# Performance work log

Hardware: AMD Instinct MI355X
Metric: run time of the kernel (lower is better)

The kernel has to match this reference:

```python
import jax, jax.numpy as jnp
import numpy as np

B, S, D = 1, 2048, 128   # batch, seq_len, num_hidden (== head dim)
H, KVH = 32, 8           # num_heads, num_kv_heads
REP = H // KVH           # num_rep = 4
D_K = 128                # softmax scale denominator sqrt(d_k)
ROPE_THETA = 10000.0


def _rope(x):
    # x: (B, h, S, D). Standard rotate-half RoPE over last dim, positions on axis -2.
    inv_freq = 1.0 / (ROPE_THETA ** (jnp.arange(0, D, 2, dtype=jnp.float32) / D))  # (D/2,)
    ang = jnp.arange(S, dtype=jnp.float32)[:, None] * inv_freq                      # (S, D/2)
    cos = jnp.concatenate([jnp.cos(ang), jnp.cos(ang)], axis=-1)                    # (S, D)
    sin = jnp.concatenate([jnp.sin(ang), jnp.sin(ang)], axis=-1)
    x1, x2 = jnp.split(x, 2, axis=-1)
    rot = jnp.concatenate([-x2, x1], axis=-1)
    return x * cos + rot * sin


def setup_inputs() -> dict:
    key = jax.random.key(0)
    ks = jax.random.split(key, 11)
    w = 0.02
    return {
        "query":  jax.random.normal(ks[0], (B, S, D), jnp.float32),
        "keys":   jax.random.normal(ks[1], (B, S, D), jnp.float32),
        "values": jax.random.normal(ks[2], (B, S, D), jnp.float32),
        "Wq": jax.random.normal(ks[3], (D, H * D), jnp.float32) * w,
        "bq": jnp.zeros((H * D,), jnp.float32),
        "Wk": jax.random.normal(ks[4], (D, KVH * D), jnp.float32) * w,
        "bk": jnp.zeros((KVH * D,), jnp.float32),
        "Wv": jax.random.normal(ks[5], (D, KVH * D), jnp.float32) * w,
        "bv": jnp.zeros((KVH * D,), jnp.float32),
        "Wo": jax.random.normal(ks[6], (H * D, D), jnp.float32) * w,
        "bo": jnp.zeros((D,), jnp.float32),
    }


def reference(query, keys, values, Wq, bq, Wk, bk, Wv, bv, Wo, bo):
    # Projections; faithful to torch .view(): plain reshape (B,S,h*D)->(B,h,S,D), no transpose.
    q = (query @ Wq + bq).reshape(B, H, S, D)
    k = (keys @ Wk + bk).reshape(B, KVH, S, D)
    v = (values @ Wv + bv).reshape(B, KVH, S, D)
    k = _rope(k)
    v = _rope(v)  # module applies RoPE to values too
    # torch repeat tiles kv heads: q head i <-> kv head (i % KVH).
    qg = q.reshape(B, REP, KVH, S, D)
    scores = jnp.einsum('brgsd,bgtd->brgst', qg, k) / jnp.sqrt(jnp.float32(D_K))
    attn = jax.nn.softmax(scores, axis=-1)  # mask=False path, no causal mask
    out = jnp.einsum('brgst,bgtd->brgsd', attn, v).reshape(B, H, S, D)
    out = out.transpose(0, 2, 1, 3).reshape(B, S, H * D)
    return out @ Wo + bo
```

## Files before the change

### kernel.cpp

```cpp
#include <hip/hip_runtime.h>
#include <math.h>


#define SCALE_L2E 0.12751878222550723f
#define L2_10K_64 0.20762050593045952f

typedef short bf16x8 __attribute__((ext_vector_type(8)));
typedef float f32x4 __attribute__((ext_vector_type(4)));
typedef float f32x16 __attribute__((ext_vector_type(16)));

__device__ __forceinline__ unsigned short f2b(float f) {
  union { float f; unsigned u; } x; x.f = f;
  return (unsigned short)((x.u + 0x7FFFu + ((x.u >> 16) & 1u)) >> 16);
}
__device__ __forceinline__ float b2f(unsigned short b) {
  union { unsigned u; float f; } x; x.u = ((unsigned)b) << 16;
  return x.f;
}
__device__ __forceinline__ void lds_dma16(void* lds, const void* g) {
  __builtin_amdgcn_global_load_lds(
      (const __attribute__((address_space(1))) unsigned int*)g,
      (__attribute__((address_space(3))) unsigned int*)lds, 16, 0, 0);
}
__device__ __forceinline__ unsigned cvtpk(float lo, float hi) {
  unsigned r;
  asm("v_cvt_pk_bf16_f32 %0, %1, %2" : "=v"(r) : "v"(lo), "v"(hi));
  return r;
}
#define PLSWAP(a, b) asm("v_permlane32_swap_b32 %0, %1" : "+v"(a), "+v"(b))

__device__ __forceinline__ void redist(unsigned pw[8], bf16x8* f0, bf16x8* f1) {
  PLSWAP(pw[0], pw[2]); PLSWAP(pw[1], pw[3]);
  PLSWAP(pw[4], pw[6]); PLSWAP(pw[5], pw[7]);
  union { unsigned u[4]; bf16x8 v; } a, b;
  a.u[0] = pw[0]; a.u[1] = pw[1]; a.u[2] = pw[2]; a.u[3] = pw[3];
  b.u[0] = pw[4]; b.u[1] = pw[5]; b.u[2] = pw[6]; b.u[3] = pw[7];
  *f0 = a.v; *f1 = b.v;
}

__global__ __launch_bounds__(256) void prep_weights(
    const float* __restrict__ Wk, const float* __restrict__ Wv,
    const float* __restrict__ Wo, const float* __restrict__ Wq,
    unsigned short* __restrict__ Wkt, unsigned short* __restrict__ Wvt,
    unsigned short* __restrict__ Wot, unsigned short* __restrict__ Wq2) {
  __shared__ unsigned short T[64][66];
  int b = blockIdx.x, tid = threadIdx.x;
  const float* W;
  unsigned short* D;
  int K, N, tk, tn;
  if (b < 32) {
    W = Wk; D = Wkt; K = 128; N = 1024; int ti = b;       tk = ti & 1;  tn = ti >> 1;
  } else if (b < 64) {
    W = Wv; D = Wvt; K = 128; N = 1024; int ti = b - 32;  tk = ti & 1;  tn = ti >> 1;
  } else if (b < 192) {
    W = Wo; D = Wot; K = 4096; N = 128; int ti = b - 64;  tk = ti >> 1; tn = ti & 1;
  } else {
    int i0 = ((b - 192) * 256 + tid) * 16;
#pragma unroll
    for (int j = 0; j < 16; ++j) Wq2[i0 + j] = f2b(Wq[i0 + j]);
    return;
  }
  int k0 = tk * 64, n0 = tn * 64;
  int c = tid & 63, q = tid >> 6;
#pragma unroll
  for (int i = 0; i < 16; ++i) {
    int r = i * 4 + q;
    T[r][c] = f2b(W[(size_t)(k0 + r) * N + n0 + c]);
  }
  __syncthreads();
#pragma unroll
  for (int i = 0; i < 16; ++i) {
    int r = i * 4 + q;
    D[(size_t)(n0 + r) * K + k0 + c] = T[c][r];
  }
}

__global__ __launch_bounds__(256) void proj_kv(
    const float* __restrict__ keys, const float* __restrict__ values,
    const unsigned short* __restrict__ Wkt, const unsigned short* __restrict__ Wvt,
    const float* __restrict__ bk, const float* __restrict__ bv,
    unsigned short* __restrict__ kp, unsigned short* __restrict__ vt) {
  int bx = blockIdx.x, m0 = blockIdx.y * 64;
  int tid = threadIdx.x;
  int w = tid >> 6, l = tid & 63;
  int l16 = l & 15, g4 = l >> 4;
  int arow = m0 + w * 16 + l16;
  const f32x4 fz = {0.f, 0.f, 0.f, 0.f};
  int vmode = bx >> 3;
  int n0 = (bx & 7) * 128, tb = bx & 7;
  const float* X = vmode ? values : keys;
  const unsigned short* Wt = vmode ? Wvt : Wkt;
  const float* bias = vmode ? bv : bk;
  f32x4 acc[8];
#pragma unroll
  for (int nb = 0; nb < 8; ++nb) acc[nb] = fz;
#pragma unroll
  for (int kc = 0; kc < 4; ++kc) {
    int kbase = kc * 32 + g4 * 8;
    const float* xp = X + (size_t)arow * 128 + kbase;
    bf16x8 a;
#pragma unroll
    for (int j = 0; j < 8; ++j) a[j] = (short)f2b(xp[j]);
#pragma unroll
    for (int nb = 0; nb < 8; ++nb) {
      bf16x8 b = *(const bf16x8*)(Wt + (size_t)(n0 + nb * 16 + l16) * 128 + kbase);
      acc[nb] = __builtin_amdgcn_mfma_f32_16x16x32_bf16(a, b, acc[nb], 0, 0, 0);
    }
  }
#pragma unroll
  for (int nb = 0; nb < 4; ++nb) {
    int d2 = nb * 16 + l16;
    float invf = exp2f(-(float)d2 * L2_10K_64);
    float blo = bias[n0 + d2], bhi = bias[n0 + d2 + 64];
#pragma unroll
    for (int r = 0; r < 4; ++r) {
      int mi = m0 + w * 16 + g4 * 4 + r;
      int t = (mi & 255) * 8 + tb;
      float ang = (float)t * invf;
      float sf, cf;
      __sincosf(ang, &sf, &cf);
      float x1 = acc[nb][r] + blo;
      float x2 = acc[nb + 4][r] + bhi;
      unsigned short lo = f2b(x1 * cf - x2 * sf);
      unsigned short hi = f2b(x2 * cf + x1 * sf);
      int g = mi >> 8;
      if (vmode) {
        vt[(size_t)g * 262144 + (size_t)d2 * 2048 + t] = lo;
        vt[(size_t)g * 262144 + (size_t)(d2 + 64) * 2048 + t] = hi;
      } else {
        kp[(size_t)g * 262144 + (size_t)t * 128 + d2] = lo;
        kp[(size_t)g * 262144 + (size_t)t * 128 + d2 + 64] = hi;
      }
    }
  }
}

__global__ void ws_marker(float* __restrict__ out) {
  out[blockIdx.x * 256 + threadIdx.x] = 12345.0f;
}

__global__ void reduce_out(const float* __restrict__ part, const float* __restrict__ bo,
                           float* __restrict__ out) {
  int idx = blockIdx.x * 256 + threadIdx.x;
  float s = bo[idx & 127];
#pragma unroll
  for (int g = 0; g < 8; ++g) s += part[(size_t)g * 262144 + idx];
  out[idx] = s;
}

__global__ __launch_bounds__(256, 2) void attn_kernel(
    const float* __restrict__ X, const unsigned short* __restrict__ Wqb,
    const float* __restrict__ bq,
    const unsigned short* __restrict__ kp, const unsigned short* __restrict__ vt,
    const unsigned short* __restrict__ Wot, float* __restrict__ part) {
  __shared__ __align__(16) char smem[65536];
  int bid = blockIdx.x;
  int g = bid & 7;
  int qi0 = (bid >> 3) * 32;
  int q5 = qi0 >> 5;
  int tid = threadIdx.x;
  int w = tid >> 6, l = tid & 63;
  int l31 = l & 31, hi = l >> 5;
  int hw = g + 8 * w;

  const f32x16 fz16 = {0.f};

  {
    unsigned short* Uni = (unsigned short*)smem;
    int col0 = tid * 16;
#pragma unroll
    for (int jp = 0; jp < 2; ++jp) {
      float acc[2][16];
#pragma unroll
      for (int j = 0; j < 2; ++j)
#pragma unroll
        for (int cc = 0; cc < 16; ++cc) acc[j][cc] = bq[col0 + cc];
      const float* xr0 = X + (size_t)((g + 8 * (jp * 2)) * 64 + q5) * 128;
      const float* xr1 = X + (size_t)((g + 8 * (jp * 2 + 1)) * 64 + q5) * 128;
      for (int k = 0; k < 128; ++k) {
        float x0 = xr0[k], x1 = xr1[k];
        bf16x8 w0 = *(const bf16x8*)(Wqb + (size_t)k * 4096 + col0);
        bf16x8 w1 = *(const bf16x8*)(Wqb + (size_t)k * 4096 + col0 + 8);
#pragma unroll
        for (int e = 0; e < 8; ++e) {
          float f0 = b2f((unsigned short)w0[e]), f1 = b2f((unsigned short)w1[e]);
          acc[0][e] += x0 * f0; acc[0][8 + e] += x0 * f1;
          acc[1][e] += x1 * f0; acc[1][8 + e] += x1 * f1;
        }
      }
#pragma unroll
      for (int j = 0; j < 2; ++j)
#pragma unroll
        for (int cc = 0; cc < 16; ++cc)
          Uni[(jp * 2 + j) * 4096 + col0 + cc] = f2b(acc[j][cc]);
    }
  }
  __syncthreads();
  bf16x8 qfrag[8];
  {
    unsigned short* Uni = (unsigned short*)smem;
#pragma unroll
    for (int kc = 0; kc < 8; ++kc)
      qfrag[kc] = *(const bf16x8*)&Uni[w * 4096 + l31 * 128 + kc * 16 + hi * 8];
  }
  __syncthreads();

  const char* kg = (const char*)(kp + (size_t)g * 262144);
  const char* vg = (const char*)(vt + (size_t)g * 262144);

#define STAGE_K(tn, kb)                                                         \
  {                                                                             \
    _Pragma("unroll") for (int i = 0; i < 4; ++i) {                             \
      int off = w * 4096 + i * 1024 + l * 16;                                   \
      int row = off >> 8, ch = (off >> 4) & 15;                                 \
      int rch = ch ^ (row & 15);                                                \
      lds_dma16(smem + (kb) * 16384 + w * 4096 + i * 1024,                      \
                kg + (size_t)(tn) * 16384 + (size_t)row * 256 + rch * 16);      \
    }                                                                           \
  }
#define STAGE_V(tn, vb)                                                         \
  {                                                                             \
    _Pragma("unroll") for (int i = 0; i < 4; ++i) {                             \
      int off = w * 4096 + i * 1024 + l * 16;                                   \
      int row = off >> 7, ch = (off >> 4) & 7;                                  \
      int rch = ch ^ (row & 7);                                                 \
      lds_dma16(smem + 32768 + (vb) * 16384 + w * 4096 + i * 1024,              \
                vg + (size_t)row * 4096 + (size_t)(tn) * 128 + rch * 16);       \
    }                                                                           \
  }

  STAGE_K(0, 0);
  STAGE_V(0, 0);
  __syncthreads();

  f32x16 oacc[4];
#pragma unroll
  for (int db = 0; db < 4; ++db) oacc[db] = fz16;
  float lacc = 0.f;

  int c = 0;
  for (int t = 0; t < 32; ++t) {
    if (t < 31) { STAGE_K(t + 1, c ^ 1); STAGE_V(t + 1, c ^ 1); }

#pragma unroll
    for (int jb = 0; jb < 2; ++jb) {
      f32x16 sacc = fz16;
      __builtin_amdgcn_s_setprio(1);
#pragma unroll
      for (int kc = 0; kc < 8; ++kc) {
        int row = jb * 32 + l31;
        int rch = (kc * 2 + hi) ^ (row & 15);
        bf16x8 kfrag = *(const bf16x8*)(smem + c * 16384 + row * 256 + rch * 16);
        sacc = __builtin_amdgcn_mfma_f32_32x32x16_bf16(kfrag, qfrag[kc], sacc, 0, 0, 0);
      }
      __builtin_amdgcn_s_setprio(0);
      float p[16];
#pragma unroll
      for (int j = 0; j < 16; ++j) {
        p[j] = exp2f(sacc[j] * SCALE_L2E);
        lacc += p[j];
      }
      unsigned pw[8];
#pragma unroll
      for (int m = 0; m < 8; ++m) pw[m] = cvtpk(p[2 * m], p[2 * m + 1]);
      bf16x8 pf0, pf1;
      redist(pw, &pf0, &pf1);
      __builtin_amdgcn_s_setprio(1);
#pragma unroll
      for (int ks = 0; ks < 2; ++ks) {
        int ksg = jb * 2 + ks;
        bf16x8 pf = ks ? pf1 : pf0;
#pragma unroll
        for (int db = 0; db < 4; ++db) {
          int row = db * 32 + l31;
          int rch = (ksg * 2 + hi) ^ (row & 7);
          bf16x8 vfrag = *(const bf16x8*)(smem + 32768 + c * 16384 + row * 128 + rch * 16);
          oacc[db] = __builtin_amdgcn_mfma_f32_32x32x16_bf16(vfrag, pf, oacc[db], 0, 0, 0);
        }
      }
      __builtin_amdgcn_s_setprio(0);
    }
    __syncthreads();
    c ^= 1;
  }

  float ltot = lacc + __shfl_xor(lacc, 32, 64);
  float invl = 1.f / ltot;

  f32x16 acc2[4];
#pragma unroll
  for (int nb = 0; nb < 4; ++nb) acc2[nb] = fz16;
  bf16x8 ofrag[8];
#pragma unroll
  for (int db = 0; db < 4; ++db) {
    unsigned pw[8];
#pragma unroll
    for (int m = 0; m < 8; ++m)
      pw[m] = cvtpk(oacc[db][2 * m] * invl, oacc[db][2 * m + 1] * invl);
    redist(pw, &ofrag[db * 2], &ofrag[db * 2 + 1]);
  }
#pragma unroll
  for (int ks = 0; ks < 8; ++ks) {
#pragma unroll
    for (int nb = 0; nb < 4; ++nb) {
      bf16x8 wof = *(const bf16x8*)(Wot + (size_t)(nb * 32 + l31) * 4096 + hw * 128 + ks * 16 + hi * 8);
      acc2[nb] = __builtin_amdgcn_mfma_f32_32x32x16_bf16(wof, ofrag[ks], acc2[nb], 0, 0, 0);
    }
  }
  __syncthreads();
  float* Psum = (float*)(smem + w * 16384);
#pragma unroll
  for (int nb = 0; nb < 4; ++nb) {
#pragma unroll
    for (int j = 0; j < 16; ++j) {
      int no = nb * 32 + (j & 3) + 8 * (j >> 2) + 4 * hi;
      Psum[l31 * 128 + no] = acc2[nb][j];
    }
  }
  __syncthreads();
  {
    float* P0 = (float*)smem;
    float* dst = part + (size_t)g * 262144 + (size_t)qi0 * 128;
#pragma unroll
    for (int i = 0; i < 16; ++i) {
      int cidx = i * 256 + tid;
      dst[cidx] = P0[cidx] + P0[4096 + cidx] + P0[8192 + cidx] + P0[12288 + cidx];
    }
  }
#undef STAGE_K
#undef STAGE_V
}

extern "C" void kernel_launch(void* const* d_in, const int* in_sizes, int n_in,
                              void* d_out, int out_size, void* d_ws, size_t ws_size,
                              hipStream_t stream) {
  const float* query  = (const float*)d_in[0];
  const float* keys   = (const float*)d_in[1];
  const float* values = (const float*)d_in[2];
  const float* Wq = (const float*)d_in[3];
  const float* bq = (const float*)d_in[4];
  const float* Wk = (const float*)d_in[5];
  const float* bk = (const float*)d_in[6];
  const float* Wv = (const float*)d_in[7];
  const float* bv = (const float*)d_in[8];
  const float* Wo = (const float*)d_in[9];
  const float* bo = (const float*)d_in[10];
  float* out = (float*)d_out;
  char* ws = (char*)d_ws;
  const size_t MB = 1024 * 1024;
  const size_t NEED = 18 * MB + 512 * 1024;
  if (ws_size < NEED) {
    ws_marker<<<1024, 256, 0, stream>>>(out);
    return;
  }
  unsigned short* Wq2   = (unsigned short*)(ws);
  unsigned short* Wkt   = (unsigned short*)(ws + 1 * MB);
  unsigned short* Wvt   = (unsigned short*)(ws + 1 * MB + 256 * 1024);
  unsigned short* Wot   = (unsigned short*)(ws + 1 * MB + 512 * 1024);
  unsigned short* kproj = (unsigned short*)(ws + 2 * MB + 512 * 1024);
  unsigned short* vt    = (unsigned short*)(ws + 6 * MB + 512 * 1024);
  float* part           = (float*)(ws + 10 * MB + 512 * 1024);

  prep_weights<<<320, 256, 0, stream>>>(Wk, Wv, Wo, Wq, Wkt, Wvt, Wot, Wq2);
  proj_kv<<<dim3(16, 32), 256, 0, stream>>>(keys, values, Wkt, Wvt, bk, bv, kproj, vt);
  attn_kernel<<<512, 256, 0, stream>>>(query, Wq2, bq, kproj, vt, Wot, part);
  reduce_out<<<1024, 256, 0, stream>>>(part, bo, out);
}
```

Before: 171.5 us.

## Split attention KV loop across wave pairs and add separate MFMA Q projection

The attention kernel grows to 512 threads, and each pair of waves splits the two 32-key halves of every KV tile. Partial outputs and row sums from the two waves are merged through LDS before the output projection. K and V staging is divided between the two groups of waves. When the workspace is large enough, the Q projection moves from scalar FMA inside the attention kernel to a separate MFMA-based proj_q kernel that writes a bf16 Q buffer, at the cost of an extra launch and a 16MB intermediate.

```diff
diff --git a/kernel.cpp b/kernel.cpp
--- a/kernel.cpp
+++ b/kernel.cpp
@@ -42,7 +42,7 @@
     const float* __restrict__ Wk, const float* __restrict__ Wv,
     const float* __restrict__ Wo, const float* __restrict__ Wq,
     unsigned short* __restrict__ Wkt, unsigned short* __restrict__ Wvt,
-    unsigned short* __restrict__ Wot, unsigned short* __restrict__ Wq2) {
+    unsigned short* __restrict__ Wot, unsigned short* __restrict__ Wq2, int big) {
   __shared__ unsigned short T[64][66];
   int b = blockIdx.x, tid = threadIdx.x;
   const float* W;
@@ -55,10 +55,13 @@
   } else if (b < 192) {
     W = Wo; D = Wot; K = 4096; N = 128; int ti = b - 64;  tk = ti >> 1; tn = ti & 1;
   } else {
-    int i0 = ((b - 192) * 256 + tid) * 16;
-#pragma unroll
-    for (int j = 0; j < 16; ++j) Wq2[i0 + j] = f2b(Wq[i0 + j]);
-    return;
+    if (!big) {
+      int i0 = ((b - 192) * 256 + tid) * 16;
+#pragma unroll
+      for (int j = 0; j < 16; ++j) Wq2[i0 + j] = f2b(Wq[i0 + j]);
+      return;
+    }
+    W = Wq; D = Wq2; K = 128; N = 4096; int ti = b - 192; tk = ti & 1;  tn = ti >> 1;
   }
   int k0 = tk * 64, n0 = tn * 64;
   int c = tid & 63, q = tid >> 6;
@@ -135,6 +138,46 @@
   }
 }
 
+__global__ __launch_bounds__(256) void proj_q(const float* __restrict__ X,
+                                              const unsigned short* __restrict__ Wqt,
+                                              const float* __restrict__ bq,
+                                              unsigned short* __restrict__ qp) {
+  int n0 = blockIdx.x * 64, m0 = blockIdx.y * 64;
+  int tid = threadIdx.x;
+  int w = tid >> 6, l = tid & 63;
+  int l16 = l & 15, g4 = l >> 4;
+  int arow = m0 + w * 16 + l16;
+  const f32x4 fz = {0.f, 0.f, 0.f, 0.f};
+  f32x4 acc[4];
+#pragma unroll
+  for (int nb = 0; nb < 4; ++nb) acc[nb] = fz;
+#pragma unroll
+  for (int kc = 0; kc < 4; ++kc) {
+    int kbase = kc * 32 + g4 * 8;
+    const float* xp = X + (size_t)arow * 128 + kbase;
+    bf16x8 a;
+#pragma unroll
+    for (int j = 0; j < 8; ++j) a[j] = (short)f2b(xp[j]);
+#pragma unroll
+    for (int nb = 0; nb < 4; ++nb) {
+      bf16x8 b = *(const bf16x8*)(Wqt + (size_t)(n0 + nb * 16 + l16) * 128 + kbase);
+      acc[nb] = __builtin_amdgcn_mfma_f32_16x16x32_bf16(a, b, acc[nb], 0, 0, 0);
+    }
+  }
+#pragma unroll
+  for (int nb = 0; nb < 4; ++nb) {
+    int n = n0 + nb * 16 + l16;
+    float bvv = bq[n];
+#pragma unroll
+    for (int r = 0; r < 4; ++r) {
+      int mi = m0 + w * 16 + g4 * 4 + r;
+      int h = mi >> 6;
+      int s = ((mi & 63) << 5) | (n >> 7);
+      qp[((size_t)h * 2048 + s) * 128 + (n & 127)] = f2b(acc[nb][r] + bvv);
+    }
+  }
+}
+
 __global__ void ws_marker(float* __restrict__ out) {
   out[blockIdx.x * 256 + threadIdx.x] = 12345.0f;
 }
@@ -148,12 +191,13 @@
   out[idx] = s;
 }
 
-__global__ __launch_bounds__(256, 2) void attn_kernel(
+template <int FUSED_Q>
+__global__ __launch_bounds__(512, 4) void attn_kernel(
     const float* __restrict__ X, const unsigned short* __restrict__ Wqb,
-    const float* __restrict__ bq,
+    const float* __restrict__ bq, const unsigned short* __restrict__ qp,
     const unsigned short* __restrict__ kp, const unsigned short* __restrict__ vt,
     const unsigned short* __restrict__ Wot, float* __restrict__ part) {
-  __shared__ __align__(16) char smem[65536];
+  __shared__ __align__(16) char smem[69632];
   int bid = blockIdx.x;
   int g = bid & 7;
   int qi0 = (bid >> 3) * 32;
@@ -161,76 +205,78 @@
   int tid = threadIdx.x;
   int w = tid >> 6, l = tid & 63;
   int l31 = l & 31, hi = l >> 5;
-  int hw = g + 8 * w;
+  int hh = w >> 1, jb = w & 1;
+  int hw = g + 8 * hh;
 
   const f32x16 fz16 = {0.f};
-
-  {
+  bf16x8 qfrag[8];
+
+  if (FUSED_Q) {
     unsigned short* Uni = (unsigned short*)smem;
-    int col0 = tid * 16;
-#pragma unroll
-    for (int jp = 0; jp < 2; ++jp) {
-      float acc[2][16];
-#pragma unroll
-      for (int j = 0; j < 2; ++j)
-#pragma unroll
-        for (int cc = 0; cc < 16; ++cc) acc[j][cc] = bq[col0 + cc];
-      const float* xr0 = X + (size_t)((g + 8 * (jp * 2)) * 64 + q5) * 128;
-      const float* xr1 = X + (size_t)((g + 8 * (jp * 2 + 1)) * 64 + q5) * 128;
+    int col0 = tid * 8;
+    {
+      float acc[4][8];
+#pragma unroll
+      for (int jj = 0; jj < 4; ++jj)
+#pragma unroll
+        for (int e = 0; e < 8; ++e) acc[jj][e] = bq[col0 + e];
+      const float* xr0 = X + (size_t)((g + 0) * 64 + q5) * 128;
+      const float* xr1 = X + (size_t)((g + 8) * 64 + q5) * 128;
+      const float* xr2 = X + (size_t)((g + 16) * 64 + q5) * 128;
+      const float* xr3 = X + (size_t)((g + 24) * 64 + q5) * 128;
       for (int k = 0; k < 128; ++k) {
-        float x0 = xr0[k], x1 = xr1[k];
+        float x0 = xr0[k], x1 = xr1[k], x2 = xr2[k], x3 = xr3[k];
         bf16x8 w0 = *(const bf16x8*)(Wqb + (size_t)k * 4096 + col0);
-        bf16x8 w1 = *(const bf16x8*)(Wqb + (size_t)k * 4096 + col0 + 8);
 #pragma unroll
         for (int e = 0; e < 8; ++e) {
-          float f0 = b2f((unsigned short)w0[e]), f1 = b2f((unsigned short)w1[e]);
-          acc[0][e] += x0 * f0; acc[0][8 + e] += x0 * f1;
-          acc[1][e] += x1 * f0; acc[1][8 + e] += x1 * f1;
+          float f0 = b2f((unsigned short)w0[e]);
+          acc[0][e] += x0 * f0; acc[1][e] += x1 * f0;
+          acc[2][e] += x2 * f0; acc[3][e] += x3 * f0;
         }
       }
 #pragma unroll
-      for (int j = 0; j < 2; ++j)
-#pragma unroll
-        for (int cc = 0; cc < 16; ++cc)
-          Uni[(jp * 2 + j) * 4096 + col0 + cc] = f2b(acc[j][cc]);
-    }
-  }
-  __syncthreads();
-  bf16x8 qfrag[8];
-  {
-    unsigned short* Uni = (unsigned short*)smem;
+      for (int jj = 0; jj < 4; ++jj)
+#pragma unroll
+        for (int e = 0; e < 8; ++e) Uni[jj * 4096 + col0 + e] = f2b(acc[jj][e]);
+    }
+    __syncthreads();
 #pragma unroll
     for (int kc = 0; kc < 8; ++kc)
-      qfrag[kc] = *(const bf16x8*)&Uni[w * 4096 + l31 * 128 + kc * 16 + hi * 8];
-  }
-  __syncthreads();
+      qfrag[kc] = *(const bf16x8*)&Uni[hh * 4096 + l31 * 128 + kc * 16 + hi * 8];
+    __syncthreads();
+  } else {
+    const unsigned short* qrow = qp + ((size_t)hw * 2048 + qi0 + l31) * 128;
+#pragma unroll
+    for (int kc = 0; kc < 8; ++kc)
+      qfrag[kc] = *(const bf16x8*)(qrow + kc * 16 + hi * 8);
+  }
 
   const char* kg = (const char*)(kp + (size_t)g * 262144);
   const char* vg = (const char*)(vt + (size_t)g * 262144);
 
-#define STAGE_K(tn, kb)                                                         \
+#define STAGE(tn, cb)                                                           \
   {                                                                             \
-    _Pragma("unroll") for (int i = 0; i < 4; ++i) {                             \
-      int off = w * 4096 + i * 1024 + l * 16;                                   \
-      int row = off >> 8, ch = (off >> 4) & 15;                                 \
-      int rch = ch ^ (row & 15);                                                \
-      lds_dma16(smem + (kb) * 16384 + w * 4096 + i * 1024,                      \
-                kg + (size_t)(tn) * 16384 + (size_t)row * 256 + rch * 16);      \
+    int w4 = w & 3;                                                             \
+    if (w < 4) {                                                                \
+      _Pragma("unroll") for (int i = 0; i < 4; ++i) {                           \
+        int off = w4 * 4096 + i * 1024 + l * 16;                                \
+        int row = off >> 8, ch = (off >> 4) & 15;                               \
+        int rch = ch ^ (row & 15);                                              \
+        lds_dma16(smem + (cb) * 16384 + w4 * 4096 + i * 1024,                   \
+                  kg + (size_t)(tn) * 16384 + (size_t)row * 256 + rch * 16);    \
+      }                                                                         \
+    } else {                                                                    \
+      _Pragma("unroll") for (int i = 0; i < 4; ++i) {                           \
+        int off = w4 * 4096 + i * 1024 + l * 16;                                \
+        int row = off >> 7, ch = (off >> 4) & 7;                                \
+        int rch = ch ^ (row & 7);                                               \
+        lds_dma16(smem + 32768 + (cb) * 16384 + w4 * 4096 + i * 1024,           \
+                  vg + (size_t)row * 4096 + (size_t)(tn) * 128 + rch * 16);     \
+      }                                                                         \
     }                                                                           \
   }
-#define STAGE_V(tn, vb)                                                         \
-  {                                                                             \
-    _Pragma("unroll") for (int i = 0; i < 4; ++i) {                             \
-      int off = w * 4096 + i * 1024 + l * 16;                                   \
-      int row = off >> 7, ch = (off >> 4) & 7;                                  \
-      int rch = ch ^ (row & 7);                                                 \
-      lds_dma16(smem + 32768 + (vb) * 16384 + w * 4096 + i * 1024,              \
-                vg + (size_t)row * 4096 + (size_t)(tn) * 128 + rch * 16);       \
-    }                                                                           \
-  }
-
-  STAGE_K(0, 0);
-  STAGE_V(0, 0);
+
+  STAGE(0, 0);
   __syncthreads();
 
   f32x16 oacc[4];
@@ -240,95 +286,113 @@
 
   int c = 0;
   for (int t = 0; t < 32; ++t) {
-    if (t < 31) { STAGE_K(t + 1, c ^ 1); STAGE_V(t + 1, c ^ 1); }
-
-#pragma unroll
-    for (int jb = 0; jb < 2; ++jb) {
-      f32x16 sacc = fz16;
-      __builtin_amdgcn_s_setprio(1);
-#pragma unroll
-      for (int kc = 0; kc < 8; ++kc) {
-        int row = jb * 32 + l31;
-        int rch = (kc * 2 + hi) ^ (row & 15);
-        bf16x8 kfrag = *(const bf16x8*)(smem + c * 16384 + row * 256 + rch * 16);
-        sacc = __builtin_amdgcn_mfma_f32_32x32x16_bf16(kfrag, qfrag[kc], sacc, 0, 0, 0);
-      }
-      __builtin_amdgcn_s_setprio(0);
-      float p[16];
-#pragma unroll
-      for (int j = 0; j < 16; ++j) {
-        p[j] = exp2f(sacc[j] * SCALE_L2E);
-        lacc += p[j];
-      }
-      unsigned pw[8];
-#pragma unroll
-      for (int m = 0; m < 8; ++m) pw[m] = cvtpk(p[2 * m], p[2 * m + 1]);
-      bf16x8 pf0, pf1;
-      redist(pw, &pf0, &pf1);
-      __builtin_amdgcn_s_setprio(1);
-#pragma unroll
-      for (int ks = 0; ks < 2; ++ks) {
-        int ksg = jb * 2 + ks;
-        bf16x8 pf = ks ? pf1 : pf0;
-#pragma unroll
-        for (int db = 0; db < 4; ++db) {
-          int row = db * 32 + l31;
-          int rch = (ksg * 2 + hi) ^ (row & 7);
-          bf16x8 vfrag = *(const bf16x8*)(smem + 32768 + c * 16384 + row * 128 + rch * 16);
-          oacc[db] = __builtin_amdgcn_mfma_f32_32x32x16_bf16(vfrag, pf, oacc[db], 0, 0, 0);
-        }
-      }
-      __builtin_amdgcn_s_setprio(0);
-    }
+    if (t < 31) STAGE(t + 1, c ^ 1);
+
+    f32x16 sacc = fz16;
+    __builtin_amdgcn_s_setprio(1);
+#pragma unroll
+    for (int kc = 0; kc < 8; ++kc) {
+      int row = jb * 32 + l31;
+      int rch = (kc * 2 + hi) ^ (row & 15);
+      bf16x8 kfrag = *(const bf16x8*)(smem + c * 16384 + row * 256 + rch * 16);
+      sacc = __builtin_amdgcn_mfma_f32_32x32x16_bf16(kfrag, qfrag[kc], sacc, 0, 0, 0);
+    }
+    __builtin_amdgcn_s_setprio(0);
+    float p[16];
+#pragma unroll
+    for (int j = 0; j < 16; ++j) {
+      p[j] = exp2f(sacc[j] * SCALE_L2E);
+      lacc += p[j];
+    }
+    unsigned pw[8];
+#pragma unroll
+    for (int m = 0; m < 8; ++m) pw[m] = cvtpk(p[2 * m], p[2 * m + 1]);
+    bf16x8 pf0, pf1;
+    redist(pw, &pf0, &pf1);
+    __builtin_amdgcn_s_setprio(1);
+#pragma unroll
+    for (int ks = 0; ks < 2; ++ks) {
+      int ksg = jb * 2 + ks;
+      bf16x8 pf = ks ? pf1 : pf0;
+#pragma unroll
+      for (int db = 0; db < 4; ++db) {
+        int row = db * 32 + l31;
+        int rch = (ksg * 2 + hi) ^ (row & 7);
+        bf16x8 vfrag = *(const bf16x8*)(smem + 32768 + c * 16384 + row * 128 + rch * 16);
+        oacc[db] = __builtin_amdgcn_mfma_f32_32x32x16_bf16(vfrag, pf, oacc[db], 0, 0, 0);
+      }
+    }
+    __builtin_amdgcn_s_setprio(0);
     __syncthreads();
     c ^= 1;
   }
 
-  float ltot = lacc + __shfl_xor(lacc, 32, 64);
-  float invl = 1.f / ltot;
-
-  f32x16 acc2[4];
-#pragma unroll
-  for (int nb = 0; nb < 4; ++nb) acc2[nb] = fz16;
-  bf16x8 ofrag[8];
-#pragma unroll
-  for (int db = 0; db < 4; ++db) {
-    unsigned pw[8];
-#pragma unroll
-    for (int m = 0; m < 8; ++m)
-      pw[m] = cvtpk(oacc[db][2 * m] * invl, oacc[db][2 * m + 1] * invl);
-    redist(pw, &ofrag[db * 2], &ofrag[db * 2 + 1]);
-  }
-#pragma unroll
-  for (int ks = 0; ks < 8; ++ks) {
-#pragma unroll
-    for (int nb = 0; nb < 4; ++nb) {
-      bf16x8 wof = *(const bf16x8*)(Wot + (size_t)(nb * 32 + l31) * 4096 + hw * 128 + ks * 16 + hi * 8);
-      acc2[nb] = __builtin_amdgcn_mfma_f32_32x32x16_bf16(wof, ofrag[ks], acc2[nb], 0, 0, 0);
-    }
+  float lw = lacc + __shfl_xor(lacc, 32, 64);
+
+  float* smemF = (float*)smem;
+  float* Ph = smemF + hh * 4224;
+  float* Laux = smemF + 4 * 4224;
+  if (jb == 0) {
+#pragma unroll
+    for (int db = 0; db < 4; ++db)
+#pragma unroll
+      for (int j = 0; j < 16; ++j) {
+        int d = db * 32 + (j & 3) + 8 * (j >> 2) + 4 * hi;
+        Ph[d * 33 + l31] = oacc[db][j];
+      }
+    if (l == 0) Laux[w] = lw;
   }
   __syncthreads();
-  float* Psum = (float*)(smem + w * 16384);
-#pragma unroll
-  for (int nb = 0; nb < 4; ++nb) {
-#pragma unroll
-    for (int j = 0; j < 16; ++j) {
-      int no = nb * 32 + (j & 3) + 8 * (j >> 2) + 4 * hi;
-      Psum[l31 * 128 + no] = acc2[nb][j];
-    }
+  if (jb == 1) {
+    float invl = 1.f / (lw + Laux[w - 1]);
+    bf16x8 ofrag[8];
+#pragma unroll
+    for (int db = 0; db < 4; ++db) {
+      float ov[16];
+#pragma unroll
+      for (int j = 0; j < 16; ++j) {
+        int d = db * 32 + (j & 3) + 8 * (j >> 2) + 4 * hi;
+        ov[j] = (Ph[d * 33 + l31] + oacc[db][j]) * invl;
+      }
+      unsigned pw[8];
+#pragma unroll
+      for (int m = 0; m < 8; ++m) pw[m] = cvtpk(ov[2 * m], ov[2 * m + 1]);
+      redist(pw, &ofrag[db * 2], &ofrag[db * 2 + 1]);
+    }
+    f32x16 acc2[4];
+#pragma unroll
+    for (int nb = 0; nb < 4; ++nb) acc2[nb] = fz16;
+#pragma unroll
+    for (int ks = 0; ks < 8; ++ks) {
+#pragma unroll
+      for (int nb = 0; nb < 4; ++nb) {
+        bf16x8 wof = *(const bf16x8*)(Wot + (size_t)(nb * 32 + l31) * 4096 + hw * 128 + ks * 16 + hi * 8);
+        acc2[nb] = __builtin_amdgcn_mfma_f32_32x32x16_bf16(wof, ofrag[ks], acc2[nb], 0, 0, 0);
+      }
+    }
+    __syncthreads();
+#pragma unroll
+    for (int nb = 0; nb < 4; ++nb)
+#pragma unroll
+      for (int j = 0; j < 16; ++j) {
+        int no = nb * 32 + (j & 3) + 8 * (j >> 2) + 4 * hi;
+        Ph[l31 * 130 + no] = acc2[nb][j];
+      }
+  } else {
+    __syncthreads();
   }
   __syncthreads();
   {
-    float* P0 = (float*)smem;
     float* dst = part + (size_t)g * 262144 + (size_t)qi0 * 128;
 #pragma unroll
-    for (int i = 0; i < 16; ++i) {
-      int cidx = i * 256 + tid;
-      dst[cidx] = P0[cidx] + P0[4096 + cidx] + P0[8192 + cidx] + P0[12288 + cidx];
-    }
-  }
-#undef STAGE_K
-#undef STAGE_V
+    for (int i = 0; i < 8; ++i) {
+      int idx = i * 512 + tid;
+      int q = idx >> 7, no = idx & 127;
+      int o = q * 130 + no;
+      dst[idx] = smemF[o] + smemF[4224 + o] + smemF[8448 + o] + smemF[12672 + o];
+    }
+  }
+#undef STAGE
 }
 
 extern "C" void kernel_launch(void* const* d_in, const int* in_sizes, int n_in,
@@ -348,21 +412,31 @@
   float* out = (float*)d_out;
   char* ws = (char*)d_ws;
   const size_t MB = 1024 * 1024;
-  const size_t NEED = 18 * MB + 512 * 1024;
-  if (ws_size < NEED) {
+  const size_t NEED_MIN = 18 * MB + 512 * 1024;
+  const size_t NEED_BIG = 34 * MB + 512 * 1024;
+  if (ws_size < NEED_MIN) {
     ws_marker<<<1024, 256, 0, stream>>>(out);
     return;
   }
+  int big = ws_size >= NEED_BIG;
   unsigned short* Wq2   = (unsigned short*)(ws);
   unsigned short* Wkt   = (unsigned short*)(ws + 1 * MB);
   unsigned short* Wvt   = (unsigned short*)(ws + 1 * MB + 256 * 1024);
   unsigned short* Wot   = (unsigned short*)(ws + 1 * MB + 512 * 1024);
   unsigned short* kproj = (unsigned short*)(ws + 2 * MB + 512 * 1024);
   unsigned short* vt    = (unsigned short*)(ws + 6 * MB + 512 * 1024);
-  float* part           = (float*)(ws + 10 * MB + 512 * 1024);
-
-  prep_weights<<<320, 256, 0, stream>>>(Wk, Wv, Wo, Wq, Wkt, Wvt, Wot, Wq2);
+  unsigned short* qproj = (unsigned short*)(ws + 10 * MB + 512 * 1024);
+  float* part = big ? (float*)(ws + 26 * MB + 512 * 1024)
+                    : (float*)(ws + 10 * MB + 512 * 1024);
+
+  prep_weights<<<320, 256, 0, stream>>>(Wk, Wv, Wo, Wq, Wkt, Wvt, Wot, Wq2, big);
   proj_kv<<<dim3(16, 32), 256, 0, stream>>>(keys, values, Wkt, Wvt, bk, bv, kproj, vt);
-  attn_kernel<<<512, 256, 0, stream>>>(query, Wq2, bq, kproj, vt, Wot, part);
+
+  if (big) {
+    proj_q<<<dim3(64, 32), 256, 0, stream>>>(query, Wq2, bq, qproj);
+    attn_kernel<0><<<512, 512, 0, stream>>>(query, Wq2, bq, qproj, kproj, vt, Wot, part);
+  } else {
+    attn_kernel<1><<<512, 512, 0, stream>>>(query, Wq2, bq, nullptr, kproj, vt, Wot, part);
+  }
   reduce_out<<<1024, 256, 0, stream>>>(part, bo, out);
 }
```

Measured after the change: 210.1 us. 22.5% more time.
